# Optimization experiments

Hardware: AMD Instinct MI355X
Metric: run time of the kernel (lower is better)

The kernel has to match this reference:

```python
import jax, jax.numpy as jnp
import numpy as np

DT = 0.0125
DX = 0.2
MU_U = 0.1
MU_V = 0.1
BETA = 1.0


def _laplace(f):
    # f: [T, Hp, Wp] -> valid 5x5 4th-order Laplacian stencil / dx^2, out [T, Hp-4, Wp-4]
    c = f[:, 2:-2, 2:-2]
    near = f[:, 1:-3, 2:-2] + f[:, 3:-1, 2:-2] + f[:, 2:-2, 1:-3] + f[:, 2:-2, 3:-1]
    far = f[:, 0:-4, 2:-2] + f[:, 4:, 2:-2] + f[:, 2:-2, 0:-4] + f[:, 2:-2, 4:]
    return (-5.0 * c + (4.0 / 3.0) * near - (1.0 / 12.0) * far) / (DX * DX)


def setup_inputs() -> dict:
    key = jax.random.key(0)
    T, C, H, W = 200, 2, 512, 512
    output = jax.random.normal(key, (T, C, H, W), dtype=jnp.float32)
    return {"output": output}


def reference(output):
    # Periodic padding: 2 on the low side, 3 on the high side, both spatial dims
    p = jnp.pad(output, ((0, 0), (0, 0), (2, 3), (2, 3)), mode="wrap")  # [T, 2, H+5, W+5]
    pu = p[:, 0]  # [T, Hp, Wp]
    pv = p[:, 1]

    # Spatial derivatives on frames [0 : T-2]
    lap_u = _laplace(pu[:-2])  # [T-2, H+1, W+1]
    lap_v = _laplace(pv[:-2])

    # Interior fields (rows/cols 2:-2 of the padded grid)
    u_full = pu[:, 2:-2, 2:-2]  # [T, H+1, W+1]
    v_full = pv[:, 2:-2, 2:-2]
    u = u_full[:-2]
    v = v_full[:-2]

    # Temporal derivative: kernel [-1, 1, 0] valid conv over time => (x[t+1]-x[t])/dt
    u_t = (u_full[1:-1] - u_full[:-2]) / DT  # [T-2, H+1, W+1]
    v_t = (v_full[1:-1] - v_full[:-2]) / DT

    s = u * u + v * v
    f_u = u_t - (MU_U * lap_u + (1.0 - s) * u + BETA * s * v)
    f_v = v_t - (MU_V * lap_v + (1.0 - s) * v - BETA * s * u)

    mse_u = jnp.mean(f_u * f_u)
    mse_v = jnp.mean(f_v * f_v)
    return (mse_u, mse_v)
```

## Files before the change

kernel.cpp:

```cpp
#include <hip/hip_runtime.h>

#define HH 512
#define WW 512
#define NQ 128
#define NT 198
#define RPB 8
#define NSTRIP (HH / RPB)
#define NBLK (NSTRIP * NT)

__global__ __launch_bounds__(128)
void pde_residual_kernel(const float* __restrict__ in, float2* __restrict__ partial) {
    const int t     = blockIdx.y;
    const int strip = blockIdx.x;
    const int q     = threadIdx.x;
    const int j0    = q * 4;
    const int i0    = strip * RPB;

    const size_t plane4 = (size_t)HH * NQ;
    const float4* __restrict__ U  = (const float4*)in + (size_t)(2 * t) * plane4;
    const float4* __restrict__ V  = U + plane4;
    const float4* __restrict__ Un = U + 2 * plane4;
    const float4* __restrict__ Vn = U + 3 * plane4;

    float4 wu[5], wv[5];
    #pragma unroll
    for (int s = 0; s < 5; ++s) {
        const int rq = ((i0 - 2 + s) & (HH - 1)) * NQ;
        wu[s] = U[rq + q];
        wv[s] = V[rq + q];
    }

    const int jl2 = ((j0 - 2) & (WW - 1)) >> 1;
    const int jr2 = ((j0 + 4) & (WW - 1)) >> 1;

    float su = 0.0f, sv = 0.0f;

    #pragma unroll
    for (int r = 0; r < RPB; ++r) {
        const int rq = ((i0 + r) & (HH - 1)) * NQ;

        const float2* __restrict__ U2 = (const float2*)(U + rq);
        const float2* __restrict__ V2 = (const float2*)(V + rq);
        const float2 uLp = U2[jl2];
        const float2 uRp = U2[jr2];
        const float2 vLp = V2[jl2];
        const float2 vRp = V2[jr2];
        const float4 unC = Un[rq + q];
        const float4 vnC = Vn[rq + q];

        float4 nu, nv;
        if (r < RPB - 1) {
            const int nrq = ((i0 + r + 3) & (HH - 1)) * NQ;
            nu = U[nrq + q];
            nv = V[nrq + q];
        }

        const float4 um2 = wu[(r + 0) % 5], vm2 = wv[(r + 0) % 5];
        const float4 um1 = wu[(r + 1) % 5], vm1 = wv[(r + 1) % 5];
        const float4 uc4 = wu[(r + 2) % 5], vc4 = wv[(r + 2) % 5];
        const float4 up1 = wu[(r + 3) % 5], vp1 = wv[(r + 3) % 5];
        const float4 up2 = wu[(r + 4) % 5], vp2 = wv[(r + 4) % 5];

        const float hu[8] = {uLp.x, uLp.y, uc4.x, uc4.y, uc4.z, uc4.w, uRp.x, uRp.y};
        const float hv[8] = {vLp.x, vLp.y, vc4.x, vc4.y, vc4.z, vc4.w, vRp.x, vRp.y};
        const float uN[4] = {um1.x + up1.x, um1.y + up1.y, um1.z + up1.z, um1.w + up1.w};
        const float uF[4] = {um2.x + up2.x, um2.y + up2.y, um2.z + up2.z, um2.w + up2.w};
        const float vN[4] = {vm1.x + vp1.x, vm1.y + vp1.y, vm1.z + vp1.z, vm1.w + vp1.w};
        const float vF[4] = {vm2.x + vp2.x, vm2.y + vp2.y, vm2.z + vp2.z, vm2.w + vp2.w};
        const float tuu[4] = {unC.x, unC.y, unC.z, unC.w};
        const float tvv[4] = {vnC.x, vnC.y, vnC.z, vnC.w};

        const float wi = (i0 + r == 0) ? 2.0f : 1.0f;

        #pragma unroll
        for (int k = 0; k < 4; ++k) {
            const float uc = hu[k + 2];
            const float vc = hv[k + 2];

            const float nearu = uN[k] + hu[k + 1] + hu[k + 3];
            const float faru  = uF[k] + hu[k] + hu[k + 4];
            const float nearv = vN[k] + hv[k + 1] + hv[k + 3];
            const float farv  = vF[k] + hv[k] + hv[k + 4];

            const float lapu = (-5.0f * uc + (4.0f / 3.0f) * nearu - (1.0f / 12.0f) * faru) * 25.0f;
            const float lapv = (-5.0f * vc + (4.0f / 3.0f) * nearv - (1.0f / 12.0f) * farv) * 25.0f;

            const float ut = (tuu[k] - uc) * 80.0f;
            const float vt = (tvv[k] - vc) * 80.0f;

            const float s  = uc * uc + vc * vc;
            const float fu = ut - (0.1f * lapu + (1.0f - s) * uc + s * vc);
            const float fv = vt - (0.1f * lapv + (1.0f - s) * vc - s * uc);

            const float w = wi * ((j0 + k == 0) ? 2.0f : 1.0f);
            su += w * fu * fu;
            sv += w * fv * fv;
        }

        if (r < RPB - 1) {
            wu[r % 5] = nu;
            wv[r % 5] = nv;
        }
    }

    #pragma unroll
    for (int off = 32; off > 0; off >>= 1) {
        su += __shfl_down(su, off);
        sv += __shfl_down(sv, off);
    }
    __shared__ float s_u[2], s_v[2];
    const int wave = threadIdx.x >> 6;
    if ((threadIdx.x & 63) == 0) { s_u[wave] = su; s_v[wave] = sv; }
    __syncthreads();
    if (threadIdx.x == 0) {
        partial[blockIdx.y * gridDim.x + blockIdx.x] =
            make_float2(s_u[0] + s_u[1], s_v[0] + s_v[1]);
    }
}

__global__ __launch_bounds__(1024)
void reduce_kernel(const float2* __restrict__ partial, float* __restrict__ out) {
    double su = 0.0, sv = 0.0;
    for (int idx = threadIdx.x; idx < NBLK; idx += 1024) {
        const float2 p = partial[idx];
        su += (double)p.x;
        sv += (double)p.y;
    }
    #pragma unroll
    for (int off = 32; off > 0; off >>= 1) {
        su += __shfl_down(su, off);
        sv += __shfl_down(sv, off);
    }
    __shared__ double d_u[16], d_v[16];
    const int wave = threadIdx.x >> 6;
    if ((threadIdx.x & 63) == 0) { d_u[wave] = su; d_v[wave] = sv; }
    __syncthreads();
    if (threadIdx.x == 0) {
        double tu = 0.0, tv = 0.0;
        #pragma unroll
        for (int wv2 = 0; wv2 < 16; ++wv2) { tu += d_u[wv2]; tv += d_v[wv2]; }
        const double denom = (double)NT * 513.0 * 513.0;
        out[0] = (float)(tu / denom);
        out[1] = (float)(tv / denom);
    }
}

extern "C" void kernel_launch(void* const* d_in, const int* in_sizes, int n_in,
                              void* d_out, int out_size, void* d_ws, size_t ws_size,
                              hipStream_t stream) {
    const float* in = (const float*)d_in[0];
    float* out = (float*)d_out;
    float2* partial = (float2*)d_ws;

    dim3 grid(NSTRIP, NT);
    pde_residual_kernel<<<grid, 128, 0, stream>>>(in, partial);
    reduce_kernel<<<1, 1024, 0, stream>>>(partial, out);
}
```

Baseline: 568.2 us.

## Block over time chunks, reusing next-frame rows as current-frame centers

```diff
diff --git a/kernel.cpp b/kernel.cpp
--- a/kernel.cpp
+++ b/kernel.cpp
@@ -6,101 +6,121 @@
 #define NT 198
 #define RPB 8
 #define NSTRIP (HH / RPB)
-#define NBLK (NSTRIP * NT)
+#define TC 6
+#define NCHUNK (NT / TC)
+#define NBLK (NSTRIP * NCHUNK)
 
 __global__ __launch_bounds__(128)
 void pde_residual_kernel(const float* __restrict__ in, float2* __restrict__ partial) {
-    const int t     = blockIdx.y;
-    const int strip = blockIdx.x;
+    const int chunk = blockIdx.y;
+    const int bx    = blockIdx.x;
+    const int strip = ((bx & 7) << 3) | (bx >> 3);
     const int q     = threadIdx.x;
     const int j0    = q * 4;
     const int i0    = strip * RPB;
+    const int t0    = chunk * TC;
 
     const size_t plane4 = (size_t)HH * NQ;
-    const float4* __restrict__ U  = (const float4*)in + (size_t)(2 * t) * plane4;
-    const float4* __restrict__ V  = U + plane4;
-    const float4* __restrict__ Un = U + 2 * plane4;
-    const float4* __restrict__ Vn = U + 3 * plane4;
 
-    float4 wu[5], wv[5];
-    #pragma unroll
-    for (int s = 0; s < 5; ++s) {
-        const int rq = ((i0 - 2 + s) & (HH - 1)) * NQ;
-        wu[s] = U[rq + q];
-        wv[s] = V[rq + q];
-    }
+    const int rq_m2 = ((i0 - 2) & (HH - 1)) * NQ + q;
+    const int rq_m1 = ((i0 - 1) & (HH - 1)) * NQ + q;
+    const int rq_p8 = ((i0 + 8) & (HH - 1)) * NQ + q;
+    const int rq_p9 = ((i0 + 9) & (HH - 1)) * NQ + q;
 
     const int jl2 = ((j0 - 2) & (WW - 1)) >> 1;
     const int jr2 = ((j0 + 4) & (WW - 1)) >> 1;
 
+    float4 cu[8], cv[8];
+    {
+        const float4* __restrict__ U0 = (const float4*)in + (size_t)(2 * t0) * plane4;
+        const float4* __restrict__ V0 = U0 + plane4;
+        #pragma unroll
+        for (int s = 0; s < 8; ++s) {
+            cu[s] = U0[(i0 + s) * NQ + q];
+            cv[s] = V0[(i0 + s) * NQ + q];
+        }
+    }
+
     float su = 0.0f, sv = 0.0f;
 
-    #pragma unroll
-    for (int r = 0; r < RPB; ++r) {
-        const int rq = ((i0 + r) & (HH - 1)) * NQ;
+    for (int tt = 0; tt < TC; ++tt) {
+        const float4* __restrict__ U  = (const float4*)in + (size_t)(2 * (t0 + tt)) * plane4;
+        const float4* __restrict__ V  = U + plane4;
+        const float4* __restrict__ Un = U + 2 * plane4;
+        const float4* __restrict__ Vn = U + 3 * plane4;
 
-        const float2* __restrict__ U2 = (const float2*)(U + rq);
-        const float2* __restrict__ V2 = (const float2*)(V + rq);
-        const float2 uLp = U2[jl2];
-        const float2 uRp = U2[jr2];
-        const float2 vLp = V2[jl2];
-        const float2 vRp = V2[jr2];
-        const float4 unC = Un[rq + q];
-        const float4 vnC = Vn[rq + q];
+        const float4 hum2 = U[rq_m2], hvm2 = V[rq_m2];
+        const float4 hum1 = U[rq_m1], hvm1 = V[rq_m1];
+        const float4 hup8 = U[rq_p8], hvp8 = V[rq_p8];
+        const float4 hup9 = U[rq_p9], hvp9 = V[rq_p9];
 
-        float4 nu, nv;
-        if (r < RPB - 1) {
-            const int nrq = ((i0 + r + 3) & (HH - 1)) * NQ;
-            nu = U[nrq + q];
-            nv = V[nrq + q];
-        }
-
-        const float4 um2 = wu[(r + 0) % 5], vm2 = wv[(r + 0) % 5];
-        const float4 um1 = wu[(r + 1) % 5], vm1 = wv[(r + 1) % 5];
-        const float4 uc4 = wu[(r + 2) % 5], vc4 = wv[(r + 2) % 5];
-        const float4 up1 = wu[(r + 3) % 5], vp1 = wv[(r + 3) % 5];
-        const float4 up2 = wu[(r + 4) % 5], vp2 = wv[(r + 4) % 5];
-
-        const float hu[8] = {uLp.x, uLp.y, uc4.x, uc4.y, uc4.z, uc4.w, uRp.x, uRp.y};
-        const float hv[8] = {vLp.x, vLp.y, vc4.x, vc4.y, vc4.z, vc4.w, vRp.x, vRp.y};
-        const float uN[4] = {um1.x + up1.x, um1.y + up1.y, um1.z + up1.z, um1.w + up1.w};
-        const float uF[4] = {um2.x + up2.x, um2.y + up2.y, um2.z + up2.z, um2.w + up2.w};
-        const float vN[4] = {vm1.x + vp1.x, vm1.y + vp1.y, vm1.z + vp1.z, vm1.w + vp1.w};
-        const float vF[4] = {vm2.x + vp2.x, vm2.y + vp2.y, vm2.z + vp2.z, vm2.w + vp2.w};
-        const float tuu[4] = {unC.x, unC.y, unC.z, unC.w};
-        const float tvv[4] = {vnC.x, vnC.y, vnC.z, vnC.w};
-
-        const float wi = (i0 + r == 0) ? 2.0f : 1.0f;
+        float4 pu0 = {0,0,0,0}, pv0 = {0,0,0,0};
+        float4 pu1 = {0,0,0,0}, pv1 = {0,0,0,0};
 
         #pragma unroll
-        for (int k = 0; k < 4; ++k) {
-            const float uc = hu[k + 2];
-            const float vc = hv[k + 2];
+        for (int r = 0; r < RPB; ++r) {
+            const int rowq = (i0 + r) * NQ;
 
-            const float nearu = uN[k] + hu[k + 1] + hu[k + 3];
-            const float faru  = uF[k] + hu[k] + hu[k + 4];
-            const float nearv = vN[k] + hv[k + 1] + hv[k + 3];
-            const float farv  = vF[k] + hv[k] + hv[k + 4];
+            const float2* __restrict__ U2 = (const float2*)(U + rowq);
+            const float2* __restrict__ V2 = (const float2*)(V + rowq);
+            const float2 uLp = U2[jl2], uRp = U2[jr2];
+            const float2 vLp = V2[jl2], vRp = V2[jr2];
 
-            const float lapu = (-5.0f * uc + (4.0f / 3.0f) * nearu - (1.0f / 12.0f) * faru) * 25.0f;
-            const float lapv = (-5.0f * vc + (4.0f / 3.0f) * nearv - (1.0f / 12.0f) * farv) * 25.0f;
+            const float4 unC = Un[rowq + q];
+            const float4 vnC = Vn[rowq + q];
 
-            const float ut = (tuu[k] - uc) * 80.0f;
-            const float vt = (tvv[k] - vc) * 80.0f;
+            const float4 um2 = (r == 0) ? hum2 : (r == 1) ? hum1 : cu[r - 2];
+            const float4 vm2 = (r == 0) ? hvm2 : (r == 1) ? hvm1 : cv[r - 2];
+            const float4 um1 = (r == 0) ? hum1 : cu[r - 1];
+            const float4 vm1 = (r == 0) ? hvm1 : cv[r - 1];
+            const float4 uc4 = cu[r],      vc4 = cv[r];
+            const float4 up1 = (r == 7) ? hup8 : cu[r + 1];
+            const float4 vp1 = (r == 7) ? hvp8 : cv[r + 1];
+            const float4 up2 = (r == 6) ? hup8 : (r == 7) ? hup9 : cu[r + 2];
+            const float4 vp2 = (r == 6) ? hvp8 : (r == 7) ? hvp9 : cv[r + 2];
 
-            const float s  = uc * uc + vc * vc;
-            const float fu = ut - (0.1f * lapu + (1.0f - s) * uc + s * vc);
-            const float fv = vt - (0.1f * lapv + (1.0f - s) * vc - s * uc);
+            const float hu[8] = {uLp.x, uLp.y, uc4.x, uc4.y, uc4.z, uc4.w, uRp.x, uRp.y};
+            const float hv[8] = {vLp.x, vLp.y, vc4.x, vc4.y, vc4.z, vc4.w, vRp.x, vRp.y};
+            const float uN[4] = {um1.x + up1.x, um1.y + up1.y, um1.z + up1.z, um1.w + up1.w};
+            const float uF[4] = {um2.x + up2.x, um2.y + up2.y, um2.z + up2.z, um2.w + up2.w};
+            const float vN[4] = {vm1.x + vp1.x, vm1.y + vp1.y, vm1.z + vp1.z, vm1.w + vp1.w};
+            const float vF[4] = {vm2.x + vp2.x, vm2.y + vp2.y, vm2.z + vp2.z, vm2.w + vp2.w};
+            const float tuu[4] = {unC.x, unC.y, unC.z, unC.w};
+            const float tvv[4] = {vnC.x, vnC.y, vnC.z, vnC.w};
 
-            const float w = wi * ((j0 + k == 0) ? 2.0f : 1.0f);
-            su += w * fu * fu;
-            sv += w * fv * fv;
+            const float wi = (i0 + r == 0) ? 2.0f : 1.0f;
+
+            #pragma unroll
+            for (int k = 0; k < 4; ++k) {
+                const float uc = hu[k + 2];
+                const float vc = hv[k + 2];
+
+                const float nearu = uN[k] + hu[k + 1] + hu[k + 3];
+                const float faru  = uF[k] + hu[k] + hu[k + 4];
+                const float nearv = vN[k] + hv[k + 1] + hv[k + 3];
+                const float farv  = vF[k] + hv[k] + hv[k + 4];
+
+                const float lapu = (-5.0f * uc + (4.0f / 3.0f) * nearu - (1.0f / 12.0f) * faru) * 25.0f;
+                const float lapv = (-5.0f * vc + (4.0f / 3.0f) * nearv - (1.0f / 12.0f) * farv) * 25.0f;
+
+                const float ut = (tuu[k] - uc) * 80.0f;
+                const float vt = (tvv[k] - vc) * 80.0f;
+
+                const float s  = uc * uc + vc * vc;
+                const float fu = ut - (0.1f * lapu + (1.0f - s) * uc + s * vc);
+                const float fv = vt - (0.1f * lapv + (1.0f - s) * vc - s * uc);
+
+                const float w = wi * ((j0 + k == 0) ? 2.0f : 1.0f);
+                su += w * fu * fu;
+                sv += w * fv * fv;
+            }
+
+            if (r >= 2) { cu[r - 2] = pu0; cv[r - 2] = pv0; }
+            pu0 = pu1; pv0 = pv1;
+            pu1 = unC; pv1 = vnC;
         }
-
-        if (r < RPB - 1) {
-            wu[r % 5] = nu;
-            wv[r % 5] = nv;
-        }
+        cu[6] = pu0; cv[6] = pv0;
+        cu[7] = pu1; cv[7] = pv1;
     }
 
     #pragma unroll
@@ -152,7 +172,7 @@
     float* out = (float*)d_out;
     float2* partial = (float2*)d_ws;
 
-    dim3 grid(NSTRIP, NT);
+    dim3 grid(NSTRIP, NCHUNK);
     pde_residual_kernel<<<grid, 128, 0, stream>>>(in, partial);
     reduce_kernel<<<1, 1024, 0, stream>>>(partial, out);
 }
```

New measurement: 627.3 us. 1.1x slower.
